# Optimization experiments

Hardware: AMD Instinct MI355X
Metric: run time of the kernel (lower is better)

## Reference

```python
import jax, jax.numpy as jnp
import numpy as np

N = 50000   # nodes
E = 600000  # edges
F = 128     # num_features
H = 128     # hidden_channels
G = 64      # graphs in batch


def setup_inputs() -> dict:
    key = jax.random.key(0)
    ks = jax.random.split(key, 12)
    x = jax.random.normal(ks[0], (N, F), dtype=jnp.float32)
    edge_index = jax.random.randint(ks[1], (2, E), 0, N, dtype=jnp.int64)
    edge_mask = jax.random.randint(ks[2], (E,), 0, 3, dtype=jnp.int64)
    batch = jnp.sort(jax.random.randint(ks[3], (N,), 0, G, dtype=jnp.int64))
    s = 0.05
    W1 = jax.random.normal(ks[4], (F, H), dtype=jnp.float32) * s
    b1 = jnp.zeros((H,), jnp.float32)
    W2 = jax.random.normal(ks[5], (H, H), dtype=jnp.float32) * s
    b2 = jnp.zeros((H,), jnp.float32)
    W3 = jax.random.normal(ks[6], (H, H), dtype=jnp.float32) * s
    b3 = jnp.zeros((H,), jnp.float32)
    Wl = jax.random.normal(ks[7], (H, 1), dtype=jnp.float32) * s
    bl = jnp.zeros((1,), jnp.float32)
    return {"x": x, "edge_index": edge_index, "edge_mask": edge_mask, "batch": batch,
            "W1": W1, "b1": b1, "W2": W2, "b2": b2, "W3": W3, "b3": b3, "Wl": Wl, "bl": bl}


def gcn_conv(x, W, b, src, dst, ew, n):
    """PyG GCNConv: add self-loops, symmetric deg^-1/2 normalization.
    ew is a {0,1} per-edge weight implementing the dynamic edge subset
    (equivalent to edge_index[:, idx] subsetting, since masked edges
    contribute neither to degree nor to aggregation)."""
    h = x @ W                                                # [n, H]
    deg = jax.ops.segment_sum(ew, dst, num_segments=n) + 1.0  # self-loop adds 1
    dinv = jax.lax.rsqrt(deg)                                # deg^-1/2
    norm = ew * dinv[src] * dinv[dst]                        # per-edge coeff
    agg = jax.ops.segment_sum(h[src] * norm[:, None], dst, num_segments=n)
    agg = agg + h * (dinv * dinv)[:, None]                   # self-loop term 1/deg_i
    return agg + b


def reference(x, edge_index, edge_mask, batch, W1, b1, W2, b2, W3, b3, Wl, bl):
    src, dst = edge_index[0], edge_index[1]
    ones = jnp.ones((E,), x.dtype)
    h = jax.nn.relu(gcn_conv(x, W1, b1, src, dst, ones, N))
    m1 = (edge_mask == 1).astype(x.dtype)
    h = jax.nn.relu(gcn_conv(h, W2, b2, src, dst, m1, N))
    m2 = (edge_mask == 2).astype(x.dtype)
    h = gcn_conv(h, W3, b3, src, dst, m2, N)
    # global_mean_pool over batch ids
    sums = jax.ops.segment_sum(h, batch, num_segments=G)        # [G, H]
    cnt = jax.ops.segment_sum(jnp.ones((N,), h.dtype), batch, num_segments=G)
    pooled = sums / jnp.clip(cnt, 1.0)[:, None]
    # dropout(p=0.3) is identity in eval mode
    return pooled @ Wl + bl
```

## Files before the change

### kernel.cpp

```cpp
#include <hip/hip_runtime.h>

#define NN 50000
#define EE 600000
#define HH 128
#define GG 64
#define NPAD 50176
#define NR 196
#define RN 256
#define NSEC3 150528
#define NRT 588
#define EPB 3072
#define SCAP 3584
#define STAGB 7168

typedef __attribute__((ext_vector_type(8))) short short8;
typedef __attribute__((ext_vector_type(4))) float f32x4;
typedef __attribute__((ext_vector_type(4))) unsigned int u32x4;

__device__ __forceinline__ float bf2f(unsigned int u16) {
    union { unsigned int i; float f; } v; v.i = u16 << 16; return v.f;
}
__device__ __forceinline__ unsigned short f2bf(float f) {
    union { float f; unsigned int i; } v; v.f = f;
    unsigned int u = v.i;
    return (unsigned short)((u + 0x7FFFu + ((u >> 16) & 1u)) >> 16);
}

__device__ __forceinline__ short8 cvt8(f32x4 lo, f32x4 hi) {
    short8 r;
    r[0] = (short)f2bf(lo[0]); r[1] = (short)f2bf(lo[1]);
    r[2] = (short)f2bf(lo[2]); r[3] = (short)f2bf(lo[3]);
    r[4] = (short)f2bf(hi[0]); r[5] = (short)f2bf(hi[1]);
    r[6] = (short)f2bf(hi[2]); r[7] = (short)f2bf(hi[3]);
    return r;
}

__global__ void k_wt3z(const float* __restrict__ W1, const float* __restrict__ W2,
                       const float* __restrict__ W3, unsigned short* __restrict__ wt,
                       float* __restrict__ sums, int* __restrict__ scnt) {
    int i = blockIdx.x * 256 + threadIdx.x;
    if (i < GG * HH) sums[i] = 0.f;
    if (i < NR) scnt[i] = 0;
    int which = i >> 14;
    int r = i & 16383;
    const float* w = (which == 0) ? W1 : (which == 1) ? W2 : W3;
    int k = r >> 7, n = r & 127;
    wt[which * 16384 + n * HH + k] = f2bf(w[r]);
}

__global__ __launch_bounds__(256) void k_part(const int* __restrict__ ei, const int* __restrict__ mask,
                                              int* __restrict__ scnt, unsigned int* __restrict__ sbuf) {
    __shared__ int bcnt[256];
    __shared__ int bcur[256];
    __shared__ int gbase[256];
    int t = threadIdx.x;
    int e0 = blockIdx.x * EPB;
    unsigned int pk[12]; int bin[12];
    bcnt[t] = 0; bcur[t] = 0;
    __syncthreads();
    #pragma unroll
    for (int j = 0; j < 12; j++) {
        int e = e0 + j * 256 + t;
        if (e < EE) {
            int s = ei[e];
            int d = ei[EE + e];
            int m = mask[e];
            pk[j] = (unsigned int)s | ((unsigned int)(d & 255) << 16) | ((unsigned int)m << 24);
            bin[j] = d >> 8;
            atomicAdd(&bcnt[bin[j]], 1);
        } else bin[j] = -1;
    }
    __syncthreads();
    int v = bcnt[t];
    gbase[t] = (v > 0) ? atomicAdd(&scnt[t], v) : 0;
    __syncthreads();
    #pragma unroll
    for (int j = 0; j < 12; j++) {
        if (bin[j] >= 0) {
            int b = bin[j];
            int pos = gbase[b] + atomicAdd(&bcur[b], 1);
            if (pos < SCAP) sbuf[(size_t)b * SCAP + pos] = pk[j];
        }
    }
}

__global__ __launch_bounds__(256) void k_cnt(const int* __restrict__ scnt,
                                             const unsigned int* __restrict__ sbuf,
                                             int* __restrict__ deg, float* __restrict__ dinv,
                                             int* __restrict__ rtot) {
    __shared__ int l0[RN], l1[RN], l2[RN];
    __shared__ int red[12];
    int t = threadIdx.x, lane = t & 63, w = t >> 6;
    int rng = blockIdx.x;
    l0[t] = 0; l1[t] = 0; l2[t] = 0;
    __syncthreads();
    int cnt = scnt[rng]; if (cnt > SCAP) cnt = SCAP;
    const unsigned int* sb = sbuf + (size_t)rng * SCAP;
    for (int i = t; i < cnt; i += 256) {
        unsigned int p = sb[i];
        int dl = (int)((p >> 16) & 255u);
        int m = (int)(p >> 24);
        atomicAdd(&l0[dl], 1);
        if (m == 1) atomicAdd(&l1[dl], 1);
        else if (m == 2) atomicAdd(&l2[dl], 1);
    }
    __syncthreads();
    int node = rng * RN + t;
    int a = l0[t], b = l1[t], c = l2[t];
    deg[node] = a;
    deg[NPAD + node] = b;
    deg[2 * NPAD + node] = c;
    dinv[node] = rsqrtf((float)a + 1.0f);
    dinv[NPAD + node] = rsqrtf((float)b + 1.0f);
    dinv[2 * NPAD + node] = rsqrtf((float)c + 1.0f);
    int sa = a, sb_ = b, sc = c;
    #pragma unroll
    for (int off = 32; off > 0; off >>= 1) {
        sa += __shfl_xor(sa, off); sb_ += __shfl_xor(sb_, off); sc += __shfl_xor(sc, off);
    }
    if (lane == 0) { red[w] = sa; red[4 + w] = sb_; red[8 + w] = sc; }
    __syncthreads();
    if (t == 0) rtot[rng] = red[0] + red[1] + red[2] + red[3];
    else if (t == 1) rtot[NR + rng] = red[4] + red[5] + red[6] + red[7];
    else if (t == 2) rtot[2 * NR + rng] = red[8] + red[9] + red[10] + red[11];
}

__global__ __launch_bounds__(1024) void k_scanR(const int* __restrict__ rtot, int* __restrict__ roff) {
    __shared__ int ws[16];
    int t = threadIdx.x, lane = t & 63, w = t >> 6;
    int v = (t < NRT) ? rtot[t] : 0;
    int x = v;
    #pragma unroll
    for (int off = 1; off < 64; off <<= 1) {
        int u = __shfl_up(x, off);
        if (lane >= off) x += u;
    }
    if (lane == 63) ws[w] = x;
    __syncthreads();
    int wo = 0;
    for (int k = 0; k < w; k++) wo += ws[k];
    if (t < NRT) roff[t] = wo + x - v;
}

__global__ __launch_bounds__(256) void k_build(const int* __restrict__ scnt,
                                               const unsigned int* __restrict__ sbuf,
                                               const int* __restrict__ deg,
                                               const int* __restrict__ roff,
                                               int* __restrict__ rp,
                                               unsigned short* __restrict__ csr) {
    __shared__ int lrp0[RN + 1], lrp1[RN + 1], lrp2[RN + 1];
    __shared__ int lc0[RN], lc1[RN], lc2[RN];
    __shared__ int wsum[12];
    __shared__ unsigned short stag[STAGB];
    int t = threadIdx.x, lane = t & 63, w = t >> 6;
    int rng = blockIdx.x;
    int vd0 = rng * RN;
    int d0 = deg[vd0 + t], d1 = deg[NPAD + vd0 + t], d2 = deg[2 * NPAD + vd0 + t];
    int x0 = d0, x1 = d1, x2 = d2;
    #pragma unroll
    for (int off = 1; off < 64; off <<= 1) {
        int u0 = __shfl_up(x0, off), u1 = __shfl_up(x1, off), u2 = __shfl_up(x2, off);
        if (lane >= off) { x0 += u0; x1 += u1; x2 += u2; }
    }
    if (lane == 63) { wsum[w] = x0; wsum[4 + w] = x1; wsum[8 + w] = x2; }
    __syncthreads();
    int wo0 = 0, wo1 = 0, wo2 = 0;
    for (int k = 0; k < w; k++) { wo0 += wsum[k]; wo1 += wsum[4 + k]; wo2 += wsum[8 + k]; }
    int e0 = wo0 + x0 - d0, e1 = wo1 + x1 - d1, e2 = wo2 + x2 - d2;
    lrp0[t] = e0; lrp1[t] = e1; lrp2[t] = e2;
    if (t == 255) { lrp0[RN] = e0 + d0; lrp1[RN] = e1 + d1; lrp2[RN] = e2 + d2; }
    lc0[t] = 0; lc1[t] = 0; lc2[t] = 0;
    int base0 = roff[rng], base1 = roff[NR + rng], base2 = roff[2 * NR + rng];
    rp[vd0 + t] = base0 + e0;
    rp[NPAD + vd0 + t] = base1 + e1;
    rp[2 * NPAD + vd0 + t] = base2 + e2;
    __syncthreads();
    int c0 = lrp0[RN], c1 = lrp1[RN], c2 = lrp2[RN];
    int cnt = scnt[rng]; if (cnt > SCAP) cnt = SCAP;
    const unsigned int* sb = sbuf + (size_t)rng * SCAP;
    for (int i = t; i < cnt; i += 256) {
        unsigned int p = sb[i];
        unsigned short src = (unsigned short)(p & 0xffffu);
        int dl = (int)((p >> 16) & 255u);
        int m = (int)(p >> 24);
        int sl = lrp0[dl] + atomicAdd(&lc0[dl], 1);
        stag[sl] = src;
        if (m == 1) { sl = c0 + lrp1[dl] + atomicAdd(&lc1[dl], 1); stag[sl] = src; }
        else if (m == 2) { sl = c0 + c1 + lrp2[dl] + atomicAdd(&lc2[dl], 1); stag[sl] = src; }
    }
    __syncthreads();
    for (int i = t; i < c0; i += 256) csr[base0 + i] = stag[i];
    for (int i = t; i < c1; i += 256) csr[base1 + i] = stag[c0 + i];
    for (int i = t; i < c2; i += 256) csr[base2 + i] = stag[c0 + c1 + i];
}

__global__ __launch_bounds__(256) void k_gemm_f(const float* __restrict__ in,
                                                const unsigned short* __restrict__ wt,
                                                const float* __restrict__ dinv,
                                                unsigned short* __restrict__ h) {
    int w = threadIdx.x >> 6, lane = threadIdx.x & 63;
    int lr = lane & 15, lg = lane >> 4;
    int rowbase = (blockIdx.x * 4 + w) * 16;
    if (rowbase >= NN) return;
    int arow = rowbase + lr;
    const f32x4* ap = (const f32x4*)(in + (size_t)arow * HH + lg * 8);
    short8 a0 = cvt8(ap[0], ap[1]);
    short8 a1 = cvt8(ap[8], ap[9]);
    short8 a2 = cvt8(ap[16], ap[17]);
    short8 a3 = cvt8(ap[24], ap[25]);
    f32x4 acc[8];
    #pragma unroll
    for (int i = 0; i < 8; i++) acc[i] = (f32x4){0.f, 0.f, 0.f, 0.f};
    const unsigned short* wbase = wt + lr * HH + lg * 8;
    #pragma unroll
    for (int nc = 0; nc < 8; nc++) {
        const short8* bp = (const short8*)(wbase + nc * 16 * HH);
        short8 b0 = bp[0], b1 = bp[4], b2 = bp[8], b3 = bp[12];
        acc[nc] = __builtin_amdgcn_mfma_f32_16x16x32_bf16(a0, b0, acc[nc], 0, 0, 0);
        acc[nc] = __builtin_amdgcn_mfma_f32_16x16x32_bf16(a1, b1, acc[nc], 0, 0, 0);
        acc[nc] = __builtin_amdgcn_mfma_f32_16x16x32_bf16(a2, b2, acc[nc], 0, 0, 0);
        acc[nc] = __builtin_amdgcn_mfma_f32_16x16x32_bf16(a3, b3, acc[nc], 0, 0, 0);
    }
    int orow = rowbase + lg * 4;
    f32x4 dv = *(const f32x4*)(dinv + orow);
    #pragma unroll
    for (int nc = 0; nc < 8; nc++) {
        #pragma unroll
        for (int j = 0; j < 4; j++) {
            h[(size_t)(orow + j) * HH + nc * 16 + lr] = f2bf(acc[nc][j] * dv[j]);
        }
    }
}

__global__ __launch_bounds__(256) void k_gemm_b(const unsigned short* __restrict__ in,
                                                const unsigned short* __restrict__ wt,
                                                const float* __restrict__ dinv,
                                                unsigned short* __restrict__ h) {
    int w = threadIdx.x >> 6, lane = threadIdx.x & 63;
    int lr = lane & 15, lg = lane >> 4;
    int rowbase = (blockIdx.x * 4 + w) * 16;
    if (rowbase >= NN) return;
    int arow = rowbase + lr;
    const short8* ap = (const short8*)(in + (size_t)arow * HH + lg * 8);
    short8 a0 = ap[0], a1 = ap[4], a2 = ap[8], a3 = ap[12];
    f32x4 acc[8];
    #pragma unroll
    for (int i = 0; i < 8; i++) acc[i] = (f32x4){0.f, 0.f, 0.f, 0.f};
    const unsigned short* wbase = wt + lr * HH + lg * 8;
    #pragma unroll
    for (int nc = 0; nc < 8; nc++) {
        const short8* bp = (const short8*)(wbase + nc * 16 * HH);
        short8 b0 = bp[0], b1 = bp[4], b2 = bp[8], b3 = bp[12];
        acc[nc] = __builtin_amdgcn_mfma_f32_16x16x32_bf16(a0, b0, acc[nc], 0, 0, 0);
        acc[nc] = __builtin_amdgcn_mfma_f32_16x16x32_bf16(a1, b1, acc[nc], 0, 0, 0);
        acc[nc] = __builtin_amdgcn_mfma_f32_16x16x32_bf16(a2, b2, acc[nc], 0, 0, 0);
        acc[nc] = __builtin_amdgcn_mfma_f32_16x16x32_bf16(a3, b3, acc[nc], 0, 0, 0);
    }
    int orow = rowbase + lg * 4;
    f32x4 dv = *(const f32x4*)(dinv + orow);
    #pragma unroll
    for (int nc = 0; nc < 8; nc++) {
        #pragma unroll
        for (int j = 0; j < 4; j++) {
            h[(size_t)(orow + j) * HH + nc * 16 + lr] = f2bf(acc[nc][j] * dv[j]);
        }
    }
}

__global__ __launch_bounds__(256) void k_agg(const unsigned short* __restrict__ h,
                                             const float* __restrict__ dinv,
                                             const unsigned short* __restrict__ csr,
                                             const int* __restrict__ rp,
                                             const float* __restrict__ bias,
                                             unsigned short* __restrict__ g,
                                             int relu) {
    int tid = threadIdx.x;
    int n = blockIdx.x * 16 + (tid >> 4);
    int l = tid & 15;
    u32x4 hv = *(const u32x4*)(h + (size_t)n * HH + l * 8);
    float acc[8];
    #pragma unroll
    for (int q = 0; q < 4; q++) {
        acc[2*q] = bf2f(hv[q] & 0xffffu);
        acc[2*q+1] = bf2f(hv[q] >> 16);
    }
    int e = rp[n], end = rp[n + 1];
    for (; e + 7 < end; e += 8) {
        int s0 = (int)csr[e],     s1 = (int)csr[e + 1], s2 = (int)csr[e + 2], s3 = (int)csr[e + 3];
        int s4 = (int)csr[e + 4], s5 = (int)csr[e + 5], s6 = (int)csr[e + 6], s7 = (int)csr[e + 7];
        u32x4 v0 = *(const u32x4*)(h + (size_t)s0 * HH + l * 8);
        u32x4 v1 = *(const u32x4*)(h + (size_t)s1 * HH + l * 8);
        u32x4 v2 = *(const u32x4*)(h + (size_t)s2 * HH + l * 8);
        u32x4 v3 = *(const u32x4*)(h + (size_t)s3 * HH + l * 8);
        u32x4 v4 = *(const u32x4*)(h + (size_t)s4 * HH + l * 8);
        u32x4 v5 = *(const u32x4*)(h + (size_t)s5 * HH + l * 8);
        u32x4 v6 = *(const u32x4*)(h + (size_t)s6 * HH + l * 8);
        u32x4 v7 = *(const u32x4*)(h + (size_t)s7 * HH + l * 8);
        #pragma unroll
        for (int q = 0; q < 4; q++) {
            acc[2*q] += bf2f(v0[q] & 0xffffu); acc[2*q+1] += bf2f(v0[q] >> 16);
            acc[2*q] += bf2f(v1[q] & 0xffffu); acc[2*q+1] += bf2f(v1[q] >> 16);
            acc[2*q] += bf2f(v2[q] & 0xffffu); acc[2*q+1] += bf2f(v2[q] >> 16);
            acc[2*q] += bf2f(v3[q] & 0xffffu); acc[2*q+1] += bf2f(v3[q] >> 16);
            acc[2*q] += bf2f(v4[q] & 0xffffu); acc[2*q+1] += bf2f(v4[q] >> 16);
            acc[2*q] += bf2f(v5[q] & 0xffffu); acc[2*q+1] += bf2f(v5[q] >> 16);
            acc[2*q] += bf2f(v6[q] & 0xffffu); acc[2*q+1] += bf2f(v6[q] >> 16);
            acc[2*q] += bf2f(v7[q] & 0xffffu); acc[2*q+1] += bf2f(v7[q] >> 16);
        }
    }
    for (; e + 3 < end; e += 4) {
        int s0 = (int)csr[e], s1 = (int)csr[e + 1], s2 = (int)csr[e + 2], s3 = (int)csr[e + 3];
        u32x4 v0 = *(const u32x4*)(h + (size_t)s0 * HH + l * 8);
        u32x4 v1 = *(const u32x4*)(h + (size_t)s1 * HH + l * 8);
        u32x4 v2 = *(const u32x4*)(h + (size_t)s2 * HH + l * 8);
        u32x4 v3 = *(const u32x4*)(h + (size_t)s3 * HH + l * 8);
        #pragma unroll
        for (int q = 0; q < 4; q++) {
            acc[2*q] += bf2f(v0[q] & 0xffffu); acc[2*q+1] += bf2f(v0[q] >> 16);
            acc[2*q] += bf2f(v1[q] & 0xffffu); acc[2*q+1] += bf2f(v1[q] >> 16);
            acc[2*q] += bf2f(v2[q] & 0xffffu); acc[2*q+1] += bf2f(v2[q] >> 16);
            acc[2*q] += bf2f(v3[q] & 0xffffu); acc[2*q+1] += bf2f(v3[q] >> 16);
        }
    }
    for (; e < end; e++) {
        int s0 = (int)csr[e];
        u32x4 v0 = *(const u32x4*)(h + (size_t)s0 * HH + l * 8);
        #pragma unroll
        for (int q = 0; q < 4; q++) {
            acc[2*q] += bf2f(v0[q] & 0xffffu); acc[2*q+1] += bf2f(v0[q] >> 16);
        }
    }
    float di = dinv[n];
    f32x4 bp0 = *(const f32x4*)(bias + l * 8);
    f32x4 bp1 = *(const f32x4*)(bias + l * 8 + 4);
    float bb[8] = {bp0[0], bp0[1], bp0[2], bp0[3], bp1[0], bp1[1], bp1[2], bp1[3]};
    #pragma unroll
    for (int q = 0; q < 8; q++) {
        acc[q] = acc[q] * di + bb[q];
        if (relu) acc[q] = fmaxf(acc[q], 0.f);
    }
    u32x4 o;
    #pragma unroll
    for (int q = 0; q < 4; q++)
        o[q] = (unsigned int)f2bf(acc[2*q]) | ((unsigned int)f2bf(acc[2*q+1]) << 16);
    *(u32x4*)(g + (size_t)n * HH + l * 8) = o;
}

__global__ __launch_bounds__(128) void k_pool_part(const unsigned short* __restrict__ g3,
                                                   const int* __restrict__ batch,
                                                   float* __restrict__ sums) {
    int t = threadIdx.x;
    int n0 = blockIdx.x * 64;
    int n1 = n0 + 64; if (n1 > NN) n1 = NN;
    int curb = batch[n0];
    float acc = 0.f;
    for (int n = n0; n < n1; n++) {
        int b = batch[n];
        if (b != curb) {
            atomicAdd(&sums[curb * HH + t], acc);
            acc = 0.f;
            curb = b;
        }
        acc += bf2f((unsigned int)g3[(size_t)n * HH + t]);
    }
    atomicAdd(&sums[curb * HH + t], acc);
}

__device__ __forceinline__ int lbound(const int* a, int n, int key) {
    int lo = 0, hi = n;
    while (lo < hi) { int mid = (lo + hi) >> 1; if (a[mid] < key) lo = mid + 1; else hi = mid; }
    return lo;
}

__global__ __launch_bounds__(128) void k_head(const float* __restrict__ sums,
                                              const int* __restrict__ batch,
                                              const float* __restrict__ Wl,
                                              const float* __restrict__ bl,
                                              float* __restrict__ out) {
    int gid = blockIdx.x;
    int t = threadIdx.x;
    int lo = lbound(batch, NN, gid);
    int hi = lbound(batch, NN, gid + 1);
    float cnt = (float)(hi - lo);
    if (cnt < 1.f) cnt = 1.f;
    float prod = (sums[gid * HH + t] / cnt) * Wl[t];
    __shared__ float sm[128];
    sm[t] = prod;
    __syncthreads();
    for (int off = 64; off > 0; off >>= 1) {
        if (t < off) sm[t] += sm[t + off];
        __syncthreads();
    }
    if (t == 0) out[gid] = sm[0] + bl[0];
}

extern "C" void kernel_launch(void* const* d_in, const int* in_sizes, int n_in,
                              void* d_out, int out_size, void* d_ws, size_t ws_size,
                              hipStream_t stream) {
    const float* x    = (const float*)d_in[0];
    const int*   ei   = (const int*)d_in[1];
    const int*   mask = (const int*)d_in[2];
    const int*   batch= (const int*)d_in[3];
    const float* W1   = (const float*)d_in[4];
    const float* b1   = (const float*)d_in[5];
    const float* W2   = (const float*)d_in[6];
    const float* b2   = (const float*)d_in[7];
    const float* W3   = (const float*)d_in[8];
    const float* b3   = (const float*)d_in[9];
    const float* Wl   = (const float*)d_in[10];
    const float* bl   = (const float*)d_in[11];
    float* out = (float*)d_out;

    char* ws = (char*)d_ws;
    unsigned short* g = (unsigned short*)(ws + 0);
    unsigned short* h = (unsigned short*)(ws + 12800000);
    unsigned short* wt1 = (unsigned short*)(ws + 25600000);
    unsigned short* wt2 = wt1 + 16384;
    unsigned short* wt3 = wt2 + 16384;
    int* deg   = (int*)(ws + 25698304);
    float* dinv= (float*)(ws + 26300416);
    int* rp    = (int*)(ws + 26902528);
    int* rtot  = (int*)(ws + 27505152);
    int* roff  = (int*)(ws + 27509248);
    int* scnt  = (int*)(ws + 27513344);
    unsigned short* csr = (unsigned short*)(ws + 27514368);
    unsigned int* sbuf = (unsigned int*)(ws + 29914368);
    float* sums = (float*)(ws + 32724224);

    float* dinv1 = dinv;
    float* dinv2 = dinv + NPAD;
    float* dinv3 = dinv + 2 * NPAD;

    dim3 b256(256);
    k_wt3z<<<dim3(192), b256, 0, stream>>>(W1, W2, W3, wt1, sums, scnt);
    k_part<<<dim3((EE + EPB - 1) / EPB), b256, 0, stream>>>(ei, mask, scnt, sbuf);
    k_cnt<<<dim3(NR), b256, 0, stream>>>(scnt, sbuf, deg, dinv, rtot);
    k_scanR<<<dim3(1), dim3(1024), 0, stream>>>(rtot, roff);
    k_build<<<dim3(NR), b256, 0, stream>>>(scnt, sbuf, deg, roff, rp, csr);

    dim3 ggrid((NN + 63) / 64);
    dim3 agrid(NN / 16);

    k_gemm_f<<<ggrid, b256, 0, stream>>>(x, wt1, dinv1, h);
    k_agg<<<agrid, b256, 0, stream>>>(h, dinv1, csr, rp, b1, g, 1);
    k_gemm_b<<<ggrid, b256, 0, stream>>>(g, wt2, dinv2, h);
    k_agg<<<agrid, b256, 0, stream>>>(h, dinv2, csr, rp + NPAD, b2, g, 1);
    k_gemm_b<<<ggrid, b256, 0, stream>>>(g, wt3, dinv3, h);
    k_agg<<<agrid, b256, 0, stream>>>(h, dinv3, csr, rp + 2 * NPAD, b3, g, 0);

    k_pool_part<<<dim3((NN + 63) / 64), dim3(128), 0, stream>>>(g, batch, sums);
    k_head<<<dim3(GG), dim3(128), 0, stream>>>(sums, batch, Wl, bl, out);
}
```

Before: 187.4 us.

## Fuse degree count, range scan and CSR build into one padded-CSR kernel

Merges the count, global range scan and CSR build kernels into a single per-range kernel. Each range now writes its CSR segment at a fixed padded offset, and per-node start/end pointers replace the compact row pointer array. This drops two kernel launches, the single-block scan and the deg round-trip through global memory. In exchange the CSR has gaps, k_agg reads two pointer arrays, and edges past the fixed per-range capacity would overflow for skewed inputs.

```diff
diff --git a/kernel.cpp b/kernel.cpp
--- a/kernel.cpp
+++ b/kernel.cpp
@@ -7,11 +7,12 @@
 #define NPAD 50176
 #define NR 196
 #define RN 256
-#define NSEC3 150528
-#define NRT 588
 #define EPB 3072
 #define SCAP 3584
 #define STAGB 7168
+#define SC12 1536
+#define CSR1OFF 702464
+#define CSR2OFF 1003520
 
 typedef __attribute__((ext_vector_type(8))) short short8;
 typedef __attribute__((ext_vector_type(4))) float f32x4;
@@ -84,15 +85,21 @@
     }
 }
 
-__global__ __launch_bounds__(256) void k_cnt(const int* __restrict__ scnt,
+__global__ __launch_bounds__(256) void k_bld(const int* __restrict__ scnt,
                                              const unsigned int* __restrict__ sbuf,
-                                             int* __restrict__ deg, float* __restrict__ dinv,
-                                             int* __restrict__ rtot) {
+                                             float* __restrict__ dinv,
+                                             int* __restrict__ rpS, int* __restrict__ rpE,
+                                             unsigned short* __restrict__ csr) {
     __shared__ int l0[RN], l1[RN], l2[RN];
-    __shared__ int red[12];
+    __shared__ int lrp0[RN], lrp1[RN], lrp2[RN];
+    __shared__ int lc0[RN], lc1[RN], lc2[RN];
+    __shared__ int wsum[12];
+    __shared__ int ctot[3];
+    __shared__ unsigned short stag[STAGB];
     int t = threadIdx.x, lane = t & 63, w = t >> 6;
     int rng = blockIdx.x;
     l0[t] = 0; l1[t] = 0; l2[t] = 0;
+    lc0[t] = 0; lc1[t] = 0; lc2[t] = 0;
     __syncthreads();
     int cnt = scnt[rng]; if (cnt > SCAP) cnt = SCAP;
     const unsigned int* sb = sbuf + (size_t)rng * SCAP;
@@ -105,79 +112,32 @@
         else if (m == 2) atomicAdd(&l2[dl], 1);
     }
     __syncthreads();
+    int a = l0[t], b = l1[t], c = l2[t];
+    int x0 = a, x1 = b, x2 = c;
+    #pragma unroll
+    for (int off = 1; off < 64; off <<= 1) {
+        int u0 = __shfl_up(x0, off), u1 = __shfl_up(x1, off), u2 = __shfl_up(x2, off);
+        if (lane >= off) { x0 += u0; x1 += u1; x2 += u2; }
+    }
+    if (lane == 63) { wsum[w] = x0; wsum[4 + w] = x1; wsum[8 + w] = x2; }
+    __syncthreads();
+    int wo0 = 0, wo1 = 0, wo2 = 0;
+    for (int k = 0; k < w; k++) { wo0 += wsum[k]; wo1 += wsum[4 + k]; wo2 += wsum[8 + k]; }
+    int e0 = wo0 + x0 - a, e1 = wo1 + x1 - b, e2 = wo2 + x2 - c;
+    lrp0[t] = e0; lrp1[t] = e1; lrp2[t] = e2;
+    if (t == 255) { ctot[0] = e0 + a; ctot[1] = e1 + b; ctot[2] = e2 + c; }
     int node = rng * RN + t;
-    int a = l0[t], b = l1[t], c = l2[t];
-    deg[node] = a;
-    deg[NPAD + node] = b;
-    deg[2 * NPAD + node] = c;
     dinv[node] = rsqrtf((float)a + 1.0f);
     dinv[NPAD + node] = rsqrtf((float)b + 1.0f);
     dinv[2 * NPAD + node] = rsqrtf((float)c + 1.0f);
-    int sa = a, sb_ = b, sc = c;
-    #pragma unroll
-    for (int off = 32; off > 0; off >>= 1) {
-        sa += __shfl_xor(sa, off); sb_ += __shfl_xor(sb_, off); sc += __shfl_xor(sc, off);
-    }
-    if (lane == 0) { red[w] = sa; red[4 + w] = sb_; red[8 + w] = sc; }
-    __syncthreads();
-    if (t == 0) rtot[rng] = red[0] + red[1] + red[2] + red[3];
-    else if (t == 1) rtot[NR + rng] = red[4] + red[5] + red[6] + red[7];
-    else if (t == 2) rtot[2 * NR + rng] = red[8] + red[9] + red[10] + red[11];
-}
-
-__global__ __launch_bounds__(1024) void k_scanR(const int* __restrict__ rtot, int* __restrict__ roff) {
-    __shared__ int ws[16];
-    int t = threadIdx.x, lane = t & 63, w = t >> 6;
-    int v = (t < NRT) ? rtot[t] : 0;
-    int x = v;
-    #pragma unroll
-    for (int off = 1; off < 64; off <<= 1) {
-        int u = __shfl_up(x, off);
-        if (lane >= off) x += u;
-    }
-    if (lane == 63) ws[w] = x;
-    __syncthreads();
-    int wo = 0;
-    for (int k = 0; k < w; k++) wo += ws[k];
-    if (t < NRT) roff[t] = wo + x - v;
-}
-
-__global__ __launch_bounds__(256) void k_build(const int* __restrict__ scnt,
-                                               const unsigned int* __restrict__ sbuf,
-                                               const int* __restrict__ deg,
-                                               const int* __restrict__ roff,
-                                               int* __restrict__ rp,
-                                               unsigned short* __restrict__ csr) {
-    __shared__ int lrp0[RN + 1], lrp1[RN + 1], lrp2[RN + 1];
-    __shared__ int lc0[RN], lc1[RN], lc2[RN];
-    __shared__ int wsum[12];
-    __shared__ unsigned short stag[STAGB];
-    int t = threadIdx.x, lane = t & 63, w = t >> 6;
-    int rng = blockIdx.x;
-    int vd0 = rng * RN;
-    int d0 = deg[vd0 + t], d1 = deg[NPAD + vd0 + t], d2 = deg[2 * NPAD + vd0 + t];
-    int x0 = d0, x1 = d1, x2 = d2;
-    #pragma unroll
-    for (int off = 1; off < 64; off <<= 1) {
-        int u0 = __shfl_up(x0, off), u1 = __shfl_up(x1, off), u2 = __shfl_up(x2, off);
-        if (lane >= off) { x0 += u0; x1 += u1; x2 += u2; }
-    }
-    if (lane == 63) { wsum[w] = x0; wsum[4 + w] = x1; wsum[8 + w] = x2; }
-    __syncthreads();
-    int wo0 = 0, wo1 = 0, wo2 = 0;
-    for (int k = 0; k < w; k++) { wo0 += wsum[k]; wo1 += wsum[4 + k]; wo2 += wsum[8 + k]; }
-    int e0 = wo0 + x0 - d0, e1 = wo1 + x1 - d1, e2 = wo2 + x2 - d2;
-    lrp0[t] = e0; lrp1[t] = e1; lrp2[t] = e2;
-    if (t == 255) { lrp0[RN] = e0 + d0; lrp1[RN] = e1 + d1; lrp2[RN] = e2 + d2; }
-    lc0[t] = 0; lc1[t] = 0; lc2[t] = 0;
-    int base0 = roff[rng], base1 = roff[NR + rng], base2 = roff[2 * NR + rng];
-    rp[vd0 + t] = base0 + e0;
-    rp[NPAD + vd0 + t] = base1 + e1;
-    rp[2 * NPAD + vd0 + t] = base2 + e2;
-    __syncthreads();
-    int c0 = lrp0[RN], c1 = lrp1[RN], c2 = lrp2[RN];
-    int cnt = scnt[rng]; if (cnt > SCAP) cnt = SCAP;
-    const unsigned int* sb = sbuf + (size_t)rng * SCAP;
+    int base0 = rng * SCAP;
+    int base1 = CSR1OFF + rng * SC12;
+    int base2 = CSR2OFF + rng * SC12;
+    rpS[node] = base0 + e0;            rpE[node] = base0 + e0 + a;
+    rpS[NPAD + node] = base1 + e1;     rpE[NPAD + node] = base1 + e1 + b;
+    rpS[2 * NPAD + node] = base2 + e2; rpE[2 * NPAD + node] = base2 + e2 + c;
+    __syncthreads();
+    int c0 = ctot[0], c1 = ctot[1], c2 = ctot[2];
     for (int i = t; i < cnt; i += 256) {
         unsigned int p = sb[i];
         unsigned short src = (unsigned short)(p & 0xffffu);
@@ -270,7 +230,8 @@
 __global__ __launch_bounds__(256) void k_agg(const unsigned short* __restrict__ h,
                                              const float* __restrict__ dinv,
                                              const unsigned short* __restrict__ csr,
-                                             const int* __restrict__ rp,
+                                             const int* __restrict__ rpS,
+                                             const int* __restrict__ rpE,
                                              const float* __restrict__ bias,
                                              unsigned short* __restrict__ g,
                                              int relu) {
@@ -284,7 +245,7 @@
         acc[2*q] = bf2f(hv[q] & 0xffffu);
         acc[2*q+1] = bf2f(hv[q] >> 16);
     }
-    int e = rp[n], end = rp[n + 1];
+    int e = rpS[n], end = rpE[n];
     for (; e + 7 < end; e += 8) {
         int s0 = (int)csr[e],     s1 = (int)csr[e + 1], s2 = (int)csr[e + 2], s3 = (int)csr[e + 3];
         int s4 = (int)csr[e + 4], s5 = (int)csr[e + 5], s6 = (int)csr[e + 6], s7 = (int)csr[e + 7];
@@ -417,15 +378,13 @@
     unsigned short* wt1 = (unsigned short*)(ws + 25600000);
     unsigned short* wt2 = wt1 + 16384;
     unsigned short* wt3 = wt2 + 16384;
-    int* deg   = (int*)(ws + 25698304);
-    float* dinv= (float*)(ws + 26300416);
-    int* rp    = (int*)(ws + 26902528);
-    int* rtot  = (int*)(ws + 27505152);
-    int* roff  = (int*)(ws + 27509248);
-    int* scnt  = (int*)(ws + 27513344);
-    unsigned short* csr = (unsigned short*)(ws + 27514368);
-    unsigned int* sbuf = (unsigned int*)(ws + 29914368);
-    float* sums = (float*)(ws + 32724224);
+    float* dinv= (float*)(ws + 25698304);
+    int* rpS   = (int*)(ws + 26300416);
+    int* rpE   = (int*)(ws + 26902528);
+    int* scnt  = (int*)(ws + 27504640);
+    unsigned short* csr = (unsigned short*)(ws + 27505664);
+    unsigned int* sbuf = (unsigned int*)(ws + 30114816);
+    float* sums = (float*)(ws + 32924672);
 
     float* dinv1 = dinv;
     float* dinv2 = dinv + NPAD;
@@ -434,19 +393,17 @@
     dim3 b256(256);
     k_wt3z<<<dim3(192), b256, 0, stream>>>(W1, W2, W3, wt1, sums, scnt);
     k_part<<<dim3((EE + EPB - 1) / EPB), b256, 0, stream>>>(ei, mask, scnt, sbuf);
-    k_cnt<<<dim3(NR), b256, 0, stream>>>(scnt, sbuf, deg, dinv, rtot);
-    k_scanR<<<dim3(1), dim3(1024), 0, stream>>>(rtot, roff);
-    k_build<<<dim3(NR), b256, 0, stream>>>(scnt, sbuf, deg, roff, rp, csr);
+    k_bld<<<dim3(NR), b256, 0, stream>>>(scnt, sbuf, dinv, rpS, rpE, csr);
 
     dim3 ggrid((NN + 63) / 64);
     dim3 agrid(NN / 16);
 
     k_gemm_f<<<ggrid, b256, 0, stream>>>(x, wt1, dinv1, h);
-    k_agg<<<agrid, b256, 0, stream>>>(h, dinv1, csr, rp, b1, g, 1);
+    k_agg<<<agrid, b256, 0, stream>>>(h, dinv1, csr, rpS, rpE, b1, g, 1);
     k_gemm_b<<<ggrid, b256, 0, stream>>>(g, wt2, dinv2, h);
-    k_agg<<<agrid, b256, 0, stream>>>(h, dinv2, csr, rp + NPAD, b2, g, 1);
+    k_agg<<<agrid, b256, 0, stream>>>(h, dinv2, csr, rpS + NPAD, rpE + NPAD, b2, g, 1);
     k_gemm_b<<<ggrid, b256, 0, stream>>>(g, wt3, dinv3, h);
-    k_agg<<<agrid, b256, 0, stream>>>(h, dinv3, csr, rp + 2 * NPAD, b3, g, 0);
+    k_agg<<<agrid, b256, 0, stream>>>(h, dinv3, csr, rpS + 2 * NPAD, rpE + 2 * NPAD, b3, g, 0);
 
     k_pool_part<<<dim3((NN + 63) / 64), dim3(128), 0, stream>>>(g, batch, sums);
     k_head<<<dim3(GG), dim3(128), 0, stream>>>(sums, batch, Wl, bl, out);
```

Result: faster. 182.5 us (-2.6%).
